# Kernel tuning notes

Measured on AMD Instinct MI355X. Metric: run time of the kernel, lower is better.

The kernel has to match this reference:

```python
import math
import jax, jax.numpy as jnp
import numpy as np

B, N, C = 4, 2048, 256
KMAX, RATIO, ITERS, H = 1024, 12.0, 3, 4
TAU, SIG_FLOOR, INIT_SIG_MIX, INIT_OFF, JIT = 1.0, 0.03, 0.1, 0.5, 1e-6
W_KL, W_ENT, W_OCC, W_COL = 0.05, 0.0, 0.5, 0.1
K_USE = min(max(1, math.ceil(N / RATIO)), KMAX)  # 171
EPS = 1e-8


def _sym(M):
    return 0.5 * (M + jnp.swapaxes(M, -1, -2))


def _l2n(x):
    return x / jnp.maximum(jnp.linalg.norm(x, axis=-1, keepdims=True), 1e-12)


def _ln(x, g, b):
    m = x.mean(-1, keepdims=True)
    v = ((x - m) ** 2).mean(-1, keepdims=True)
    return (x - m) / jnp.sqrt(v + 1e-5) * g + b


def setup_inputs():
    key = jax.random.key(0)
    ks = jax.random.split(key, 16)
    s = jax.random.normal(ks[0], (B, N, C), jnp.float32)
    mu = jax.random.normal(ks[1], (B, N, 3), jnp.float32)
    # per-point SPD covariances (Sigma must be PSD for the overlap solve)
    L = jax.random.normal(ks[2], (B, N, 3, 3), jnp.float32) * 0.3
    Sigma = L @ jnp.swapaxes(L, -1, -2) + 0.05 * jnp.eye(3, dtype=jnp.float32)
    mask = jnp.ones((B, N), jnp.float32)
    lim = 1.0 / math.sqrt(C)
    u = lambda k, sh: jax.random.uniform(k, sh, jnp.float32, -lim, lim)
    return dict(
        s=s, mu=mu, Sigma=Sigma, mask=mask,
        slot_embed_pool=jax.random.normal(ks[3], (KMAX, C), jnp.float32) * 0.02,
        geo_offsets_pool=jax.random.normal(ks[4], (KMAX, 3), jnp.float32) * 0.5,
        gating_W=u(ks[5], (C, C)), proj_q_W=u(ks[6], (C, C)), proj_k_W=u(ks[7], (C, C)),
        gru_w_ih=u(ks[8], (3 * C, C)), gru_w_hh=u(ks[9], (3 * C, C)),
        gru_b_ih=u(ks[10], (3 * C,)), gru_b_hh=u(ks[11], (3 * C,)),
        ln_g=jnp.ones((C,), jnp.float32), ln_b=jnp.zeros((C,), jnp.float32),
        mlp_w1=u(ks[12], (4 * C, C)), mlp_b1=u(ks[13], (4 * C,)),
        mlp_w2=u(ks[14], (C, 4 * C)), mlp_b2=u(ks[15], (C,)),
        w_geo=jnp.float32(1.0),
        geo_scale_raw=jnp.full((H,), -4.0, jnp.float32),
        geo_bias=jnp.full((H,), -6.0, jnp.float32),
    )


def _forward(s, mu, Sigma, mask, slot_embed_pool, geo_offsets_pool, gating_W,
             proj_q_W, proj_k_W, gru_w_ih, gru_w_hh, gru_b_ih, gru_b_hh,
             ln_g, ln_b, mlp_w1, mlp_b1, mlp_w2, mlp_b2,
             w_geo, geo_scale_raw, geo_bias):
    I3 = jnp.eye(3, dtype=s.dtype)
    m1 = mask[:, :, None]                    # [B,N,1]
    cnt = jnp.maximum(mask.sum(1), EPS)      # [B]

    # ---- slot selection (eval mode: no gate noise, rand_slots=0) ----
    s_global = (s * m1).sum(1) / cnt[:, None]
    q = _l2n(s_global @ gating_W.T)
    kn = _l2n(slot_embed_pool)
    scores = q @ kn.T                        # [B,KMAX]
    idx = jax.lax.top_k(scores, K_USE)[1]    # [B,K]
    slots = slot_embed_pool[idx]             # [B,K,C]
    geo_off = geo_offsets_pool[idx]          # [B,K,3]

    # ---- masked mean/std of mu ----
    mean = (mu * m1).sum(1) / cnt[:, None]   # [B,3]
    dm = mu - mean[:, None, :]
    cov = jnp.einsum('bni,bnj->bij', dm * m1, dm) / cnt[:, None, None]
    cov = _sym(cov)
    std = jnp.sqrt(jnp.maximum(jnp.diagonal(cov, axis1=-2, axis2=-1), EPS))
    std = jnp.maximum(std, SIG_FLOOR)
    mu_k = mean[:, None, :] + geo_off * (INIT_OFF * std[:, None, :])

    Sig_avg = _sym((Sigma * m1[..., None]).sum(1) / cnt[:, None, None])
    Sig_k = jnp.broadcast_to(Sig_avg[:, None] * INIT_SIG_MIX, (B, K_USE, 3, 3))
    Sig_k = Sig_k + (SIG_FLOOR ** 2) * I3 + JIT * I3

    k_sem = s @ proj_k_W.T                   # [B,N,C]
    a_h = jax.nn.softplus(geo_scale_raw)     # [H]
    A = None
    for _ in range(ITERS):
        q_sem = slots @ proj_q_W.T           # [B,K,C]
        logits_sem = jnp.einsum('bnc,bkc->bnk', k_sem, q_sem) / math.sqrt(C)
        delta = mu[:, :, None, :] - mu_k[:, None, :, :]       # [B,N,K,3]
        sig_sum = Sigma[:, :, None] + Sig_k[:, None]          # [B,N,K,3,3]
        sol = jnp.linalg.solve(sig_sum, delta[..., None])[..., 0]
        maha = (delta * sol).sum(-1)
        logdet = jnp.linalg.slogdet(sig_sum)[1]
        G = -0.5 * (maha + logdet)                            # [B,N,K]
        geo = (a_h[None, :, None, None] * G[:, None] + geo_bias[None, :, None, None]).sum(1)
        logits = (logits_sem + w_geo * geo) / max(TAU, 1e-6)
        logits = jnp.where(m1 < 0.5, -1e9, logits)
        A = jax.nn.softmax(logits, axis=-1) * m1              # [B,N,K]
        # moment-matching merge (A already mask-weighted; matches torch A*mask)
        occ = jnp.maximum(A.sum(1), EPS)                      # [B,K]
        mu_k = jnp.einsum('bnk,bni->bki', A, mu) / occ[..., None]
        d = mu[:, :, None, :] - mu_k[:, None, :, :]
        outer = d[..., :, None] * d[..., None, :]             # [B,N,K,3,3]
        Sig_k = (jnp.einsum('bnk,bnij->bkij', A, Sigma)
                 + jnp.einsum('bnk,bnkij->bkij', A, outer)) / occ[:, :, None, None]
        Sig_k = _sym(Sig_k) + max(JIT, 1e-6) * I3
        dg = jnp.diagonal(Sig_k, axis1=-2, axis2=-1)
        dg_f = jnp.maximum(dg, SIG_FLOOR ** 2)
        Sig_k = Sig_k - I3 * dg[..., None, :] + I3 * dg_f[..., None, :]
        Sig_k = _sym(Sig_k) + JIT * I3
        denom = jnp.maximum(A.sum(1), 1e-8)
        slot_in = jnp.einsum('bnk,bnc->bkc', A, s) / denom[..., None]
        # GRU cell
        x = slot_in.reshape(-1, C)
        h = slots.reshape(-1, C)
        gi = x @ gru_w_ih.T + gru_b_ih
        gh = h @ gru_w_hh.T + gru_b_hh
        r = jax.nn.sigmoid(gi[:, :C] + gh[:, :C])
        z = jax.nn.sigmoid(gi[:, C:2 * C] + gh[:, C:2 * C])
        n = jnp.tanh(gi[:, 2 * C:] + r * gh[:, 2 * C:])
        slots = ((1.0 - z) * n + z * h).reshape(B, K_USE, C)
        xm = _ln(slots, ln_g, ln_b)
        slots = slots + (jax.nn.gelu(xm @ mlp_w1.T + mlp_b1, approximate=False) @ mlp_w2.T + mlp_b2)

    # ---- losses ----
    hist = jnp.zeros((KMAX,), jnp.float32).at[idx.reshape(-1)].add(1.0)
    p = hist / jnp.maximum(hist.sum(), 1.0)
    pc = jnp.maximum(p, 1e-8)
    usage_kl = (pc * (jnp.log(pc) - math.log(1.0 / KMAX))).sum()
    usage_neg_ent = (pc * jnp.log(pc)).sum()
    occ2 = (A * m1).sum(1)
    occ2 = occ2 / jnp.maximum(occ2.sum(-1, keepdims=True), 1e-8)
    occ_mse = ((occ2 - 1.0 / K_USE) ** 2).mean()
    X = jnp.swapaxes(A * m1, 1, 2)           # [B,K,N]
    Xn = X / jnp.maximum(jnp.linalg.norm(X, axis=-1, keepdims=True), 1e-8)
    Gm = jnp.einsum('bkn,bln->bkl', Xn, Xn)
    eyeK = jnp.eye(K_USE, dtype=A.dtype)[None]
    off = (Gm - eyeK) * (1.0 - eyeK)
    col = (off ** 2).mean()
    total = W_KL * usage_kl + W_ENT * usage_neg_ent + W_OCC * occ_mse + W_COL * col
    return (A, slots, mu_k, Sig_k, idx, usage_kl, usage_neg_ent, occ_mse, col, total)


def reference(s, mu, Sigma, mask, slot_embed_pool, geo_offsets_pool, gating_W,
              proj_q_W, proj_k_W, gru_w_ih, gru_w_hh, gru_b_ih, gru_b_hh,
              ln_g, ln_b, mlp_w1, mlp_b1, mlp_w2, mlp_b2,
              w_geo, geo_scale_raw, geo_bias):
    return _forward(s, mu, Sigma, mask, slot_embed_pool, geo_offsets_pool, gating_W,
                    proj_q_W, proj_k_W, gru_w_ih, gru_w_hh, gru_b_ih, gru_b_hh,
                    ln_g, ln_b, mlp_w1, mlp_b1, mlp_w2, mlp_b2,
                    w_geo, geo_scale_raw, geo_bias)
```

## Files before the change

### kernel.cpp

```cpp
#include <hip/hip_runtime.h>
#include <math.h>

#define B_ 4
#define N_ 2048
#define C_ 256
#define KMAX_ 1024
#define KU_ 171
#define ITERS_ 3
#define H_ 4
#define EPS_ 1e-8f
#define SIGF_ 0.03f
#define JIT_ 1e-6f
#define LOGKMAX_ 6.93147180559945f

#define WS_CNT 0
#define WS_MUS 4
#define WS_MOS 16
#define WS_SGS 40
#define WS_COLACC 100
#define WS_SSUM 128
#define WS_STATS_BYTES (1152*4)
#define WS_MEAN 1152
#define WS_STD 1164
#define WS_SIGAVG 1176
#define WS_IDXI 1216
#define WS_KSEM 1920
#define WS_QSEM (WS_KSEM+2097152)
#define WS_OCC  (WS_QSEM+175104)
#define WS_PART (WS_OCC+704)
#define WS_TAIL (WS_PART+1400832)
#define WS_QV     WS_TAIL
#define WS_SCORE (WS_TAIL+1024)
#define WS_ACPART (WS_TAIL+8192)
#define WS_ATA (WS_TAIL+700416)

#define O_A 0
#define O_SLOTS 1400832
#define O_MUK   1575936
#define O_SIGK  1577988
#define O_IDX   1584144
#define O_KL    1584828
#define O_ENT   1584829
#define O_OCC   1584830
#define O_COL   1584831
#define O_TOT   1584832

__device__ __forceinline__ float wred(float v) {
  #pragma unroll
  for (int i = 32; i; i >>= 1) v += __shfl_xor(v, i);
  return v;
}
__device__ __forceinline__ float wmax(float v) {
  #pragma unroll
  for (int i = 32; i; i >>= 1) v = fmaxf(v, __shfl_xor(v, i));
  return v;
}

__device__ __forceinline__ float blk_red(float v, float* red, int t) {
  red[t] = v; __syncthreads();
  #pragma unroll
  for (int s = 128; s > 0; s >>= 1) {
    if (t < s) red[t] += red[t + s];
    __syncthreads();
  }
  float r = red[0]; __syncthreads();
  return r;
}

__global__ __launch_bounds__(256) void k_stats(const float* __restrict__ s,
    const float* __restrict__ mu, const float* __restrict__ Sigma,
    const float* __restrict__ mask, float* __restrict__ ws) {
  int blk = blockIdx.x; int b = blk / 8; int nc = blk % 8; int t = threadIdx.x;
  int n = nc * 256 + t;
  float m = mask[b * N_ + n];
  const float* mun = mu + ((size_t)(b * N_ + n)) * 3;
  float m0 = mun[0], m1v = mun[1], m2 = mun[2];
  const float* sgn = Sigma + ((size_t)(b * N_ + n)) * 9;
  float sg[9];
  #pragma unroll
  for (int j = 0; j < 9; j++) sg[j] = sgn[j];
  int lane = t & 63;
  float vals[19];
  vals[0] = m; vals[1] = m * m0; vals[2] = m * m1v; vals[3] = m * m2;
  vals[4] = m * m0 * m0; vals[5] = m * m0 * m1v; vals[6] = m * m0 * m2;
  vals[7] = m * m1v * m1v; vals[8] = m * m1v * m2; vals[9] = m * m2 * m2;
  #pragma unroll
  for (int j = 0; j < 9; j++) vals[10 + j] = m * sg[j];
  #pragma unroll
  for (int j = 0; j < 19; j++) {
    float v = wred(vals[j]);
    if (lane == 0) {
      int base = (j == 0) ? WS_CNT + b : (j < 4 ? WS_MUS + b * 3 + (j - 1)
                 : (j < 10 ? WS_MOS + b * 6 + (j - 4) : WS_SGS + b * 9 + (j - 10)));
      atomicAdd(ws + base, v);
    }
  }
  const float* sb = s + ((size_t)b * N_ + nc * 256) * C_;
  const float* mk = mask + b * N_ + nc * 256;
  float sa = 0.f;
  #pragma unroll 4
  for (int nn = 0; nn < 256; nn++) sa += mk[nn] * sb[(size_t)nn * C_ + t];
  atomicAdd(ws + WS_SSUM + b * C_ + t, sa);
}

__global__ __launch_bounds__(64) void k_fin(float* __restrict__ ws) {
  int t = threadIdx.x;
  if (t < B_) {
    int b = t;
    float cnt = fmaxf(ws[WS_CNT + b], EPS_);
    float me[3];
    #pragma unroll
    for (int i = 0; i < 3; i++) { me[i] = ws[WS_MUS + b * 3 + i] / cnt; ws[WS_MEAN + b * 3 + i] = me[i]; }
    const int dg[3] = {0, 3, 5};
    #pragma unroll
    for (int i = 0; i < 3; i++) {
      float cov = ws[WS_MOS + b * 6 + dg[i]] / cnt - me[i] * me[i];
      ws[WS_STD + b * 3 + i] = fmaxf(sqrtf(fmaxf(cov, EPS_)), SIGF_);
    }
    #pragma unroll
    for (int i = 0; i < 3; i++)
      #pragma unroll
      for (int j = 0; j < 3; j++)
        ws[WS_SIGAVG + b * 9 + i * 3 + j] =
            0.5f * (ws[WS_SGS + b * 9 + i * 3 + j] + ws[WS_SGS + b * 9 + j * 3 + i]) / cnt;
  }
}

__global__ __launch_bounds__(256) void k_qv(const float* __restrict__ ws_ssum,
    const float* __restrict__ gW, float* __restrict__ qv_o) {
  int b = blockIdx.x, t = threadIdx.x;
  __shared__ float sb[C_];
  __shared__ float rv[256];
  sb[t] = ws_ssum[b * C_ + t];
  __syncthreads();
  const float4* g4 = (const float4*)(gW + (size_t)t * C_);
  float qr = 0.f;
  #pragma unroll 4
  for (int c4 = 0; c4 < 64; c4++) {
    float4 g = g4[c4];
    qr += sb[c4 * 4] * g.x + sb[c4 * 4 + 1] * g.y + sb[c4 * 4 + 2] * g.z + sb[c4 * 4 + 3] * g.w;
  }
  float n2 = blk_red(qr * qr, rv, t);
  qv_o[b * C_ + t] = qr / fmaxf(sqrtf(n2), 1e-12f);
}

__global__ __launch_bounds__(256) void k_score(const float* __restrict__ qv,
    const float* __restrict__ pool, float* __restrict__ score) {
  int blk = blockIdx.x; int b = blk >> 4; int pc = blk & 15;
  int t = threadIdx.x; int row = pc * 64 + (t >> 2); int q = t & 3;
  __shared__ float qs[C_];
  qs[t] = qv[b * C_ + t];
  __syncthreads();
  const float4* p4 = (const float4*)(pool + (size_t)row * C_ + q * 64);
  float d = 0.f, p2 = 0.f;
  #pragma unroll
  for (int i = 0; i < 16; i++) {
    float4 pv = p4[i];
    int c = q * 64 + i * 4;
    d += qs[c] * pv.x + qs[c + 1] * pv.y + qs[c + 2] * pv.z + qs[c + 3] * pv.w;
    p2 += pv.x * pv.x + pv.y * pv.y + pv.z * pv.z + pv.w * pv.w;
  }
  d += __shfl_xor(d, 1); d += __shfl_xor(d, 2);
  p2 += __shfl_xor(p2, 1); p2 += __shfl_xor(p2, 2);
  if (q == 0) score[b * KMAX_ + row] = d / fmaxf(sqrtf(p2), 1e-12f);
}

__global__ __launch_bounds__(256) void k_sort(const float* __restrict__ score,
    int* __restrict__ idx_o, float* __restrict__ idxf_o) {
  int b = blockIdx.x, t = threadIdx.x;
  __shared__ float val[KMAX_]; __shared__ int id[KMAX_];
  for (int j = t; j < KMAX_; j += 256) { val[j] = score[b * KMAX_ + j]; id[j] = j; }
  __syncthreads();
  for (int kk = 2; kk <= KMAX_; kk <<= 1) {
    for (int j = kk >> 1; j > 0; j >>= 1) {
      for (int i = t; i < KMAX_; i += 256) {
        int ix = i ^ j;
        if (ix > i) {
          float va = val[i], vb = val[ix]; int ia = id[i], ib = id[ix];
          bool bBeforeA = (vb > va) || (vb == va && ib < ia);
          bool up = ((i & kk) == 0);
          if (up == bBeforeA) {
            val[i] = vb; val[ix] = va; id[i] = ib; id[ix] = ia;
          }
        }
      }
      __syncthreads();
    }
  }
  if (t < KU_) {
    idx_o[b * KU_ + t] = id[t];
    idxf_o[b * KU_ + t] = (float)id[t];
  }
}

__global__ __launch_bounds__(256) void k_init(const int* __restrict__ idx,
    const float* __restrict__ pool, const float* __restrict__ geop,
    const float* __restrict__ ws, float* __restrict__ slots,
    float* __restrict__ mu_k, float* __restrict__ sig_k) {
  int blk = blockIdx.x; int b = blk / KU_, k = blk % KU_; int t = threadIdx.x;
  int j = idx[b * KU_ + k];
  slots[((size_t)(b * KU_ + k)) * C_ + t] = pool[(size_t)j * C_ + t];
  if (t < 3) {
    mu_k[(b * KU_ + k) * 3 + t] = ws[WS_MEAN + b * 3 + t] + geop[j * 3 + t] * (0.5f * ws[WS_STD + b * 3 + t]);
  }
  if (t < 9) {
    float v = ws[WS_SIGAVG + b * 9 + t] * 0.1f;
    if (t == 0 || t == 4 || t == 8) v += SIGF_ * SIGF_ + JIT_;
    sig_k[((size_t)(b * KU_ + k)) * 9 + t] = v;
  }
}

template<int ROWS>
__global__ __launch_bounds__(256) void k_gemm_plain(const float* __restrict__ in,
    const float* __restrict__ W, float* __restrict__ out, int IN, int OUT, float scale) {
  extern __shared__ float sm[];
  int t = threadIdx.x; int r0 = blockIdx.x * ROWS;
  int C4 = IN >> 2;
  for (int i = t; i < ROWS * C4; i += 256) {
    int rr = i / C4;
    ((float4*)sm)[i] = ((const float4*)(in + (size_t)(r0 + rr) * IN))[i - rr * C4];
  }
  __syncthreads();
  const float4* W4 = (const float4*)(W + (size_t)t * IN);
  const float4* sm4 = (const float4*)sm;
  float acc[ROWS];
  #pragma unroll
  for (int a = 0; a < ROWS; a++) acc[a] = 0.f;
  for (int c4 = 0; c4 < C4; c4++) {
    float4 wv = W4[c4];
    #pragma unroll
    for (int a = 0; a < ROWS; a++) {
      float4 sv = sm4[a * C4 + c4];
      acc[a] += sv.x * wv.x + sv.y * wv.y + sv.z * wv.z + sv.w * wv.w;
    }
  }
  #pragma unroll
  for (int a = 0; a < ROWS; a++)
    out[(size_t)(r0 + a) * OUT + t] = acc[a] * scale;
}

__global__ __launch_bounds__(256) void k_lgsm(const float* __restrict__ ksem,
    const float* __restrict__ qsem, const float* __restrict__ mu,
    const float* __restrict__ Sigma, const float* __restrict__ mask,
    const float* __restrict__ mu_k, const float* __restrict__ sig_k,
    const float* __restrict__ wgeo, const float* __restrict__ gsr,
    const float* __restrict__ gbias, float* __restrict__ A) {
  __shared__ float ksm[16 * C_];
  __shared__ float Asm[16][172];
  __shared__ float muk[KU_ * 3];
  __shared__ float sgk[KU_ * 6];
  __shared__ float rowd[16][10];
  int blk = blockIdx.x; int b = blk / (N_ / 16); int nt = blk % (N_ / 16);
  int t = threadIdx.x; int r0 = nt * 16;
  for (int i = t; i < 16 * (C_ >> 2); i += 256) {
    int rr = i >> 6;
    ((float4*)ksm)[i] = ((const float4*)(ksem + ((size_t)(b * N_ + r0 + rr)) * C_))[i & 63];
  }
  for (int i = t; i < KU_ * 3; i += 256) muk[i] = mu_k[(size_t)b * KU_ * 3 + i];
  for (int i = t; i < KU_ * 6; i += 256) {
    int k = i / 6, c = i % 6;
    const int map[6] = {0, 1, 2, 4, 5, 8};
    sgk[i] = sig_k[((size_t)(b * KU_ + k)) * 9 + map[c]];
  }
  if (t < 160) {
    int rr = t / 10, c = t % 10;
    int n = r0 + rr;
    float v;
    if (c == 0) v = mask[b * N_ + n];
    else if (c < 4) v = mu[((size_t)(b * N_ + n)) * 3 + (c - 1)];
    else {
      const int map[6] = {0, 1, 2, 4, 5, 8};
      v = Sigma[((size_t)(b * N_ + n)) * 9 + map[c - 4]];
    }
    rowd[rr][c] = v;
  }
  __syncthreads();
  if (t < KU_) {
    const float4* q4 = (const float4*)(qsem + ((size_t)(b * KU_ + t)) * C_);
    const float4* sm4 = (const float4*)ksm;
    float acc[16];
    #pragma unroll
    for (int a = 0; a < 16; a++) acc[a] = 0.f;
    for (int c4 = 0; c4 < 64; c4++) {
      float4 qv = q4[c4];
      #pragma unroll
      for (int a = 0; a < 16; a++) {
        float4 sv = sm4[a * 64 + c4];
        acc[a] += sv.x * qv.x + sv.y * qv.y + sv.z * qv.z + sv.w * qv.w;
      }
    }
    float ah = 0.f, bs = 0.f;
    #pragma unroll
    for (int h = 0; h < H_; h++) {
      float x = gsr[h];
      ah += fmaxf(x, 0.f) + log1pf(expf(-fabsf(x)));
      bs += gbias[h];
    }
    float wg = wgeo[0];
    float mk0 = muk[t * 3], mk1 = muk[t * 3 + 1], mk2 = muk[t * 3 + 2];
    float k00 = sgk[t * 6], k01 = sgk[t * 6 + 1], k02 = sgk[t * 6 + 2];
    float k11 = sgk[t * 6 + 3], k12 = sgk[t * 6 + 4], k22 = sgk[t * 6 + 5];
    #pragma unroll
    for (int a = 0; a < 16; a++) {
      float m = rowd[a][0];
      float d0 = rowd[a][1] - mk0, d1 = rowd[a][2] - mk1, d2 = rowd[a][3] - mk2;
      float s00 = rowd[a][4] + k00, s01 = rowd[a][5] + k01, s02 = rowd[a][6] + k02;
      float s11 = rowd[a][7] + k11, s12 = rowd[a][8] + k12, s22 = rowd[a][9] + k22;
      float c00 = s11 * s22 - s12 * s12;
      float c01 = s02 * s12 - s01 * s22;
      float c02 = s01 * s12 - s02 * s11;
      float det = s00 * c00 + s01 * c01 + s02 * c02;
      float c11 = s00 * s22 - s02 * s02;
      float c12 = s01 * s02 - s00 * s12;
      float c22 = s00 * s11 - s01 * s01;
      float inv = 1.0f / det;
      float x0 = (c00 * d0 + c01 * d1 + c02 * d2) * inv;
      float x1 = (c01 * d0 + c11 * d1 + c12 * d2) * inv;
      float x2 = (c02 * d0 + c12 * d1 + c22 * d2) * inv;
      float maha = d0 * x0 + d1 * x1 + d2 * x2;
      float logdet = logf(fmaxf(det, 1e-30f));
      float G = -0.5f * (maha + logdet);
      float l = acc[a] * 0.0625f + wg * (ah * G + bs);
      if (m < 0.5f) l = -1e9f;
      Asm[a][t] = l;
    }
  }
  __syncthreads();
  int w = t >> 6, lane = t & 63;
  #pragma unroll
  for (int q = 0; q < 4; q++) {
    int a = w * 4 + q;
    float v0 = (lane < KU_) ? Asm[a][lane] : -INFINITY;
    float v1 = (lane + 64 < KU_) ? Asm[a][lane + 64] : -INFINITY;
    float v2 = (lane + 128 < KU_) ? Asm[a][lane + 128] : -INFINITY;
    float mx = wmax(fmaxf(v0, fmaxf(v1, v2)));
    float e0 = (lane < KU_) ? expf(v0 - mx) : 0.f;
    float e1 = (lane + 64 < KU_) ? expf(v1 - mx) : 0.f;
    float e2 = (lane + 128 < KU_) ? expf(v2 - mx) : 0.f;
    float ss = wred(e0 + e1 + e2);
    float scale = rowd[a][0] / ss;
    if (lane < KU_) Asm[a][lane] = e0 * scale;
    if (lane + 64 < KU_) Asm[a][lane + 64] = e1 * scale;
    if (lane + 128 < KU_) Asm[a][lane + 128] = e2 * scale;
  }
  __syncthreads();
  for (int i = t; i < 16 * KU_; i += 256) {
    int a = i / KU_, k = i - a * KU_;
    A[((size_t)(b * N_ + r0 + a)) * KU_ + k] = Asm[a][k];
  }
}

#define AC_NC 4
__global__ __launch_bounds__(256) void k_accum_part(const float* __restrict__ A,
    const float* __restrict__ mu, const float* __restrict__ Sigma,
    float* __restrict__ part) {
  int blk = blockIdx.x;
  int nc = blk & 3; int tmp = blk >> 2; int kt = tmp % 11; int b = tmp / 11;
  int t = threadIdx.x; int nn = t >> 4; int kk = t & 15;
  int k = kt * 16 + kk;
  float S[10];
  #pragma unroll
  for (int i = 0; i < 10; i++) S[i] = 0.f;
  __shared__ float rowd[16][10];
  const int NCH = N_ / AC_NC;
  for (int n0 = nc * NCH; n0 < nc * NCH + NCH; n0 += 16) {
    __syncthreads();
    if (t < 144) {
      int rr = t / 9, c = t % 9;
      int n = n0 + rr;
      float v;
      if (c < 3) v = mu[((size_t)(b * N_ + n)) * 3 + c];
      else {
        const int map[6] = {0, 1, 2, 4, 5, 8};
        v = Sigma[((size_t)(b * N_ + n)) * 9 + map[c - 3]];
      }
      rowd[rr][c] = v;
    }
    float a = (k < KU_) ? A[((size_t)(b * N_ + n0 + nn)) * KU_ + k] : 0.f;
    __syncthreads();
    float m0 = rowd[nn][0], m1 = rowd[nn][1], m2 = rowd[nn][2];
    float g0 = rowd[nn][3], g1 = rowd[nn][4], g2 = rowd[nn][5];
    float g4 = rowd[nn][6], g5 = rowd[nn][7], g8 = rowd[nn][8];
    S[0] += a; S[1] += a * m0; S[2] += a * m1; S[3] += a * m2;
    S[4] += a * (g0 + m0 * m0); S[5] += a * (g1 + m0 * m1); S[6] += a * (g2 + m0 * m2);
    S[7] += a * (g4 + m1 * m1); S[8] += a * (g5 + m1 * m2); S[9] += a * (g8 + m2 * m2);
  }
  #pragma unroll
  for (int i = 0; i < 10; i++) { S[i] += __shfl_xor(S[i], 16); S[i] += __shfl_xor(S[i], 32); }
  __shared__ float red[4][16][10];
  int w = t >> 6, lane = t & 63;
  if (lane < 16) {
    #pragma unroll
    for (int i = 0; i < 10; i++) red[w][lane][i] = S[i];
  }
  __syncthreads();
  if (t < 160) {
    int k2 = t / 10, i = t % 10;
    float v = red[0][k2][i] + red[1][k2][i] + red[2][k2][i] + red[3][k2][i];
    part[(((size_t)nc * B_ + b) * 176 + kt * 16 + k2) * 10 + i] = v;
  }
}

__global__ __launch_bounds__(256) void k_accum_fin(const float* __restrict__ part,
    float* __restrict__ occ, float* __restrict__ mu_k, float* __restrict__ sig_k) {
  int i = blockIdx.x * 256 + threadIdx.x;
  if (i >= B_ * KU_) return;
  int b = i / KU_, k = i % KU_;
  float p[10];
  #pragma unroll
  for (int j = 0; j < 10; j++) {
    float v = 0.f;
    #pragma unroll
    for (int nc = 0; nc < AC_NC; nc++)
      v += part[(((size_t)nc * B_ + b) * 176 + k) * 10 + j];
    p[j] = v;
  }
  float o = p[0];
  occ[b * KU_ + k] = o;
  float oc = fmaxf(o, EPS_);
  float s1x = p[1], s1y = p[2], s1z = p[3];
  float q0 = s1x / oc, q1 = s1y / oc, q2 = s1z / oc;
  mu_k[(b * KU_ + k) * 3 + 0] = q0;
  mu_k[(b * KU_ + k) * 3 + 1] = q1;
  mu_k[(b * KU_ + k) * 3 + 2] = q2;
  float v00 = (p[4] - 2.f * q0 * s1x + o * q0 * q0) / oc + JIT_;
  float v01 = (p[5] - q0 * s1y - s1x * q1 + o * q0 * q1) / oc;
  float v02 = (p[6] - q0 * s1z - s1x * q2 + o * q0 * q2) / oc;
  float v11 = (p[7] - 2.f * q1 * s1y + o * q1 * q1) / oc + JIT_;
  float v12 = (p[8] - q1 * s1z - s1y * q2 + o * q1 * q2) / oc;
  float v22 = (p[9] - 2.f * q2 * s1z + o * q2 * q2) / oc + JIT_;
  v00 = fmaxf(v00, SIGF_ * SIGF_) + JIT_;
  v11 = fmaxf(v11, SIGF_ * SIGF_) + JIT_;
  v22 = fmaxf(v22, SIGF_ * SIGF_) + JIT_;
  float* po = sig_k + ((size_t)(b * KU_ + k)) * 9;
  po[0] = v00; po[1] = v01; po[2] = v02;
  po[3] = v01; po[4] = v11; po[5] = v12;
  po[6] = v02; po[7] = v12; po[8] = v22;
}

__global__ __launch_bounds__(256) void k_atn_s(const float* __restrict__ A,
    const float* __restrict__ X, float* __restrict__ part) {
  int blk = blockIdx.x;
  int nc = blk & 7; int tmp = blk >> 3; int kt = tmp % 11; int b = tmp / 11;
  int t = threadIdx.x; int k0 = kt * 16;
  __shared__ float Ach[64 * 16];
  float acc[16];
  #pragma unroll
  for (int j = 0; j < 16; j++) acc[j] = 0.f;
  for (int n0 = nc * 256; n0 < nc * 256 + 256; n0 += 64) {
    __syncthreads();
    for (int i = t; i < 64 * 16; i += 256) {
      int nn = i >> 4, kk = i & 15; int k = k0 + kk;
      Ach[i] = (k < KU_) ? A[((size_t)(b * N_ + n0 + nn)) * KU_ + k] : 0.f;
    }
    __syncthreads();
    for (int nn = 0; nn < 64; nn++) {
      float xv = X[((size_t)(b * N_ + n0 + nn)) * C_ + t];
      #pragma unroll
      for (int j = 0; j < 16; j++) acc[j] += Ach[(nn << 4) + j] * xv;
    }
  }
  #pragma unroll
  for (int j = 0; j < 16; j++) {
    int k = k0 + j;
    if (k < KU_) part[((size_t)nc * (B_ * KU_) + b * KU_ + k) * C_ + t] = acc[j];
  }
}

__global__ __launch_bounds__(256) void k_atn(const float* __restrict__ A,
    const float* __restrict__ X, float* __restrict__ out, int NX) {
  int blk = blockIdx.x;
  int nc = blk & 7; int tmp = blk >> 3; int kt = tmp % 11; int b = tmp / 11;
  int t = threadIdx.x; int k0 = kt * 16;
  __shared__ float Ach[64 * 16];
  float acc[16];
  #pragma unroll
  for (int j = 0; j < 16; j++) acc[j] = 0.f;
  for (int n0 = nc * 256; n0 < nc * 256 + 256; n0 += 64) {
    __syncthreads();
    for (int i = t; i < 64 * 16; i += 256) {
      int nn = i >> 4, kk = i & 15; int k = k0 + kk;
      Ach[i] = (k < KU_) ? A[((size_t)(b * N_ + n0 + nn)) * KU_ + k] : 0.f;
    }
    __syncthreads();
    if (t < NX) {
      for (int nn = 0; nn < 64; nn++) {
        float xv = X[((size_t)(b * N_ + n0 + nn)) * NX + t];
        #pragma unroll
        for (int j = 0; j < 16; j++) acc[j] += Ach[(nn << 4) + j] * xv;
      }
    }
  }
  if (t < NX) {
    #pragma unroll
    for (int j = 0; j < 16; j++) {
      int k = k0 + j;
      if (k < KU_) atomicAdd(&out[((size_t)(b * KU_ + k)) * NX + t], acc[j]);
    }
  }
}

__global__ __launch_bounds__(256) void k_slotup(const float* __restrict__ part,
    const float* __restrict__ occ, float* __restrict__ slots,
    const float* __restrict__ wih, const float* __restrict__ bih,
    const float* __restrict__ whh, const float* __restrict__ bhh,
    const float* __restrict__ lng, const float* __restrict__ lnb,
    const float* __restrict__ w1p, const float* __restrict__ b1p,
    const float* __restrict__ w2p, const float* __restrict__ b2p,
    const float* __restrict__ qWp, float* __restrict__ qsem) {
  __shared__ float sx[1024], sh[1024], sg[1024], sxm[1024], shid[4096];
  int t = threadIdx.x; int r0 = blockIdx.x * 4;
  for (int i = t; i < 1024; i += 256) {
    int rr = i >> 8, c = i & 255;
    int r = r0 + rr;
    float v = 0.f;
    #pragma unroll
    for (int nc = 0; nc < 8; nc++) v += part[((size_t)nc * (B_ * KU_) + r) * C_ + c];
    sx[i] = v / fmaxf(occ[r], 1e-8f);
    sh[i] = slots[(size_t)r * C_ + c];
  }
  __syncthreads();
  {
    const float4* wir = (const float4*)(wih + (size_t)t * C_);
    const float4* wiz = (const float4*)(wih + (size_t)(t + 256) * C_);
    const float4* win = (const float4*)(wih + (size_t)(t + 512) * C_);
    const float4* whr = (const float4*)(whh + (size_t)t * C_);
    const float4* whz = (const float4*)(whh + (size_t)(t + 256) * C_);
    const float4* whn = (const float4*)(whh + (size_t)(t + 512) * C_);
    const float4* sx4 = (const float4*)sx;
    const float4* sh4 = (const float4*)sh;
    float gir[4] = {0,0,0,0}, giz[4] = {0,0,0,0}, gin[4] = {0,0,0,0};
    float ghr[4] = {0,0,0,0}, ghz[4] = {0,0,0,0}, ghn[4] = {0,0,0,0};
    for (int c4 = 0; c4 < 64; c4++) {
      float4 a1 = wir[c4], a2 = wiz[c4], a3 = win[c4];
      float4 h1 = whr[c4], h2 = whz[c4], h3 = whn[c4];
      #pragma unroll
      for (int a = 0; a < 4; a++) {
        float4 xv = sx4[a * 64 + c4], hv = sh4[a * 64 + c4];
        gir[a] += xv.x * a1.x + xv.y * a1.y + xv.z * a1.z + xv.w * a1.w;
        giz[a] += xv.x * a2.x + xv.y * a2.y + xv.z * a2.z + xv.w * a2.w;
        gin[a] += xv.x * a3.x + xv.y * a3.y + xv.z * a3.z + xv.w * a3.w;
        ghr[a] += hv.x * h1.x + hv.y * h1.y + hv.z * h1.z + hv.w * h1.w;
        ghz[a] += hv.x * h2.x + hv.y * h2.y + hv.z * h2.z + hv.w * h2.w;
        ghn[a] += hv.x * h3.x + hv.y * h3.y + hv.z * h3.z + hv.w * h3.w;
      }
    }
    float bir = bih[t], biz = bih[t + 256], bin = bih[t + 512];
    float bhr = bhh[t], bhz = bhh[t + 256], bhn = bhh[t + 512];
    #pragma unroll
    for (int a = 0; a < 4; a++) {
      float r = 1.f / (1.f + expf(-(gir[a] + bir + ghr[a] + bhr)));
      float z = 1.f / (1.f + expf(-(giz[a] + biz + ghz[a] + bhz)));
      float n = tanhf(gin[a] + bin + r * (ghn[a] + bhn));
      sg[a * 256 + t] = (1.f - z) * n + z * sh[a * 256 + t];
    }
  }
  __syncthreads();
  {
    int w = t >> 6, lane = t & 63;
    int a = w;
    float x0 = sg[a * 256 + lane], x1 = sg[a * 256 + lane + 64];
    float x2 = sg[a * 256 + lane + 128], x3 = sg[a * 256 + lane + 192];
    float mean = wred(x0 + x1 + x2 + x3) * (1.f / 256.f);
    float d0 = x0 - mean, d1 = x1 - mean, d2 = x2 - mean, d3 = x3 - mean;
    float var = wred(d0 * d0 + d1 * d1 + d2 * d2 + d3 * d3) * (1.f / 256.f);
    float rstd = rsqrtf(var + 1e-5f);
    sxm[a * 256 + lane]       = d0 * rstd * lng[lane]       + lnb[lane];
    sxm[a * 256 + lane + 64]  = d1 * rstd * lng[lane + 64]  + lnb[lane + 64];
    sxm[a * 256 + lane + 128] = d2 * rstd * lng[lane + 128] + lnb[lane + 128];
    sxm[a * 256 + lane + 192] = d3 * rstd * lng[lane + 192] + lnb[lane + 192];
  }
  __syncthreads();
  {
    const float4* q0 = (const float4*)(w1p + (size_t)t * C_);
    const float4* q1 = (const float4*)(w1p + (size_t)(t + 256) * C_);
    const float4* q2 = (const float4*)(w1p + (size_t)(t + 512) * C_);
    const float4* q3 = (const float4*)(w1p + (size_t)(t + 768) * C_);
    const float4* sxm4 = (const float4*)sxm;
    float acc[4][4];
    #pragma unroll
    for (int a = 0; a < 4; a++)
      #pragma unroll
      for (int j = 0; j < 4; j++) acc[a][j] = 0.f;
    for (int c4 = 0; c4 < 64; c4++) {
      float4 v0 = q0[c4], v1 = q1[c4], v2 = q2[c4], v3 = q3[c4];
      #pragma unroll
      for (int a = 0; a < 4; a++) {
        float4 xv = sxm4[a * 64 + c4];
        acc[a][0] += xv.x * v0.x + xv.y * v0.y + xv.z * v0.z + xv.w * v0.w;
        acc[a][1] += xv.x * v1.x + xv.y * v1.y + xv.z * v1.z + xv.w * v1.w;
        acc[a][2] += xv.x * v2.x + xv.y * v2.y + xv.z * v2.z + xv.w * v2.w;
        acc[a][3] += xv.x * v3.x + xv.y * v3.y + xv.z * v3.z + xv.w * v3.w;
      }
    }
    float bb0 = b1p[t], bb1 = b1p[t + 256], bb2v = b1p[t + 512], bb3 = b1p[t + 768];
    #pragma unroll
    for (int a = 0; a < 4; a++) {
      float v;
      v = acc[a][0] + bb0; shid[a * 1024 + t]       = 0.5f * v * (1.f + erff(v * 0.70710678118654752f));
      v = acc[a][1] + bb1; shid[a * 1024 + t + 256] = 0.5f * v * (1.f + erff(v * 0.70710678118654752f));
      v = acc[a][2] + bb2v; shid[a * 1024 + t + 512] = 0.5f * v * (1.f + erff(v * 0.70710678118654752f));
      v = acc[a][3] + bb3; shid[a * 1024 + t + 768] = 0.5f * v * (1.f + erff(v * 0.70710678118654752f));
    }
  }
  __syncthreads();
  {
    const float4* wr = (const float4*)(w2p + (size_t)t * 1024);
    const float4* sh4 = (const float4*)shid;
    float o[4] = {0, 0, 0, 0};
    for (int c4 = 0; c4 < 256; c4++) {
      float4 wv = wr[c4];
      #pragma unroll
      for (int a = 0; a < 4; a++) {
        float4 hv = sh4[a * 256 + c4];
        o[a] += hv.x * wv.x + hv.y * wv.y + hv.z * wv.z + hv.w * wv.w;
      }
    }
    float bb = b2p[t];
    #pragma unroll
    for (int a = 0; a < 4; a++) {
      float fin = sg[a * 256 + t] + o[a] + bb;
      slots[(size_t)(r0 + a) * C_ + t] = fin;
      sx[a * 256 + t] = fin;
    }
  }
  __syncthreads();
  {
    const float4* qr = (const float4*)(qWp + (size_t)t * C_);
    const float4* sx4 = (const float4*)sx;
    float o[4] = {0, 0, 0, 0};
    for (int c4 = 0; c4 < 64; c4++) {
      float4 wv = qr[c4];
      #pragma unroll
      for (int a = 0; a < 4; a++) {
        float4 xv = sx4[a * 64 + c4];
        o[a] += xv.x * wv.x + xv.y * wv.y + xv.z * wv.z + xv.w * wv.w;
      }
    }
    #pragma unroll
    for (int a = 0; a < 4; a++)
      qsem[(size_t)(r0 + a) * C_ + t] = o[a];
  }
}

__global__ __launch_bounds__(256) void k_hist(const int* __restrict__ idx,
    float* __restrict__ okl, float* __restrict__ oent) {
  __shared__ float hist[KMAX_];
  int t = threadIdx.x;
  for (int i = t; i < KMAX_; i += 256) hist[i] = 0.f;
  __syncthreads();
  for (int i = t; i < B_ * KU_; i += 256) atomicAdd(&hist[idx[i]], 1.0f);
  __syncthreads();
  float kl = 0.f, ent = 0.f;
  const float tot = (float)(B_ * KU_);
  for (int i = t; i < KMAX_; i += 256) {
    float pc = fmaxf(hist[i] / tot, 1e-8f);
    float lp = logf(pc);
    kl += pc * (lp + LOGKMAX_);
    ent += pc * lp;
  }
  __shared__ float red[256];
  kl = blk_red(kl, red, t); ent = blk_red(ent, red, t);
  if (t == 0) { okl[0] = kl; oent[0] = ent; }
}

__global__ __launch_bounds__(256) void k_occmse(const float* __restrict__ occ,
    float* __restrict__ out) {
  __shared__ float so[B_ * KU_];
  int t = threadIdx.x;
  for (int i = t; i < B_ * KU_; i += 256) so[i] = occ[i];
  __syncthreads();
  __shared__ float red[256];
  __shared__ float bsum[B_];
  for (int b = 0; b < B_; b++) {
    float s = 0.f;
    for (int i = t; i < KU_; i += 256) s += so[b * KU_ + i];
    s = blk_red(s, red, t);
    if (t == 0) bsum[b] = fmaxf(s, 1e-8f);
    __syncthreads();
  }
  float acc = 0.f;
  const float invK = 1.0f / (float)KU_;
  for (int i = t; i < B_ * KU_; i += 256) {
    int b = i / KU_;
    float v = so[i] / bsum[b] - invK;
    acc += v * v;
  }
  acc = blk_red(acc, red, t);
  if (t == 0) out[0] = acc / (float)(B_ * KU_);
}

__global__ __launch_bounds__(256) void k_colpart(const float* __restrict__ AtA,
    float* __restrict__ colacc) {
  int blk = blockIdx.x; int b = blk / KU_, k = blk % KU_; int t = threadIdx.x;
  float acc = 0.f;
  if (t < KU_ && t != k) {
    float dk = AtA[((size_t)(b * KU_ + k)) * KU_ + k];
    float dt = AtA[((size_t)(b * KU_ + t)) * KU_ + t];
    float v  = AtA[((size_t)(b * KU_ + k)) * KU_ + t];
    float gm = v / (fmaxf(sqrtf(dk), 1e-8f) * fmaxf(sqrtf(dt), 1e-8f));
    acc = gm * gm;
  }
  float v = wred(acc);
  __shared__ float p[4];
  if ((t & 63) == 0) p[t >> 6] = v;
  __syncthreads();
  if (t == 0) atomicAdd(colacc, p[0] + p[1] + p[2] + p[3]);
}

__global__ void k_colfin(const float* __restrict__ colacc,
    const float* __restrict__ okl, const float* __restrict__ oent,
    const float* __restrict__ oocc, float* __restrict__ ocol, float* __restrict__ otot) {
  float col = colacc[0] / (float)(B_ * KU_ * KU_);
  ocol[0] = col;
  otot[0] = 0.05f * okl[0] + 0.0f * oent[0] + 0.5f * oocc[0] + 0.1f * col;
}

extern "C" void kernel_launch(void* const* d_in, const int* in_sizes, int n_in,
                              void* d_out_v, int out_size, void* d_ws, size_t ws_size,
                              hipStream_t stream) {
  const float* s     = (const float*)d_in[0];
  const float* mu    = (const float*)d_in[1];
  const float* Sigma = (const float*)d_in[2];
  const float* mask  = (const float*)d_in[3];
  const float* pool  = (const float*)d_in[4];
  const float* geop  = (const float*)d_in[5];
  const float* gW    = (const float*)d_in[6];
  const float* qW    = (const float*)d_in[7];
  const float* kW    = (const float*)d_in[8];
  const float* wih   = (const float*)d_in[9];
  const float* whh   = (const float*)d_in[10];
  const float* bih   = (const float*)d_in[11];
  const float* bhh   = (const float*)d_in[12];
  const float* lng   = (const float*)d_in[13];
  const float* lnb   = (const float*)d_in[14];
  const float* w1    = (const float*)d_in[15];
  const float* b1    = (const float*)d_in[16];
  const float* w2    = (const float*)d_in[17];
  const float* b2    = (const float*)d_in[18];
  const float* wgeo  = (const float*)d_in[19];
  const float* gsr   = (const float*)d_in[20];
  const float* gbias = (const float*)d_in[21];

  float* out = (float*)d_out_v;
  float* A     = out + O_A;
  float* slots = out + O_SLOTS;
  float* muk   = out + O_MUK;
  float* sigk  = out + O_SIGK;
  float* idxf  = out + O_IDX;
  float* okl   = out + O_KL;
  float* oent  = out + O_ENT;
  float* oocc  = out + O_OCC;
  float* ocol  = out + O_COL;
  float* otot  = out + O_TOT;

  float* ws = (float*)d_ws;
  int*   idxi   = (int*)(ws + WS_IDXI);
  float* ksem   = ws + WS_KSEM;
  float* qsem   = ws + WS_QSEM;
  float* occ    = ws + WS_OCC;
  float* atpart = ws + WS_PART;
  float* acpart = ws + WS_ACPART;
  float* ata    = ws + WS_ATA;
  float* colacc = ws + WS_COLACC;

  hipMemsetAsync(ws, 0, WS_STATS_BYTES, stream);
  k_stats<<<B_ * 8, 256, 0, stream>>>(s, mu, Sigma, mask, ws);
  k_fin<<<1, 64, 0, stream>>>(ws);
  k_qv<<<B_, 256, 0, stream>>>(ws + WS_SSUM, gW, ws + WS_QV);
  k_score<<<B_ * 16, 256, 0, stream>>>(ws + WS_QV, pool, ws + WS_SCORE);
  k_sort<<<B_, 256, 0, stream>>>(ws + WS_SCORE, idxi, idxf);
  k_init<<<B_ * KU_, 256, 0, stream>>>(idxi, pool, geop, ws, slots, muk, sigk);

  k_gemm_plain<8><<<1024, 256, 8 * C_ * 4, stream>>>(s, kW, ksem, C_, C_, 1.0f);
  k_gemm_plain<4><<<171, 256, 4 * C_ * 4, stream>>>(slots, qW, qsem, C_, C_, 1.0f);

  for (int it = 0; it < ITERS_; ++it) {
    k_lgsm<<<B_ * (N_ / 16), 256, 0, stream>>>(ksem, qsem, mu, Sigma, mask,
                                               muk, sigk, wgeo, gsr, gbias, A);
    k_accum_part<<<B_ * 11 * AC_NC, 256, 0, stream>>>(A, mu, Sigma, acpart);
    k_accum_fin<<<3, 256, 0, stream>>>(acpart, occ, muk, sigk);
    k_atn_s<<<B_ * 11 * 8, 256, 0, stream>>>(A, s, atpart);
    k_slotup<<<171, 256, 0, stream>>>(atpart, occ, slots, wih, bih, whh, bhh,
                                      lng, lnb, w1, b1, w2, b2, qW, qsem);
  }

  hipMemsetAsync(ata, 0, (size_t)B_ * KU_ * KU_ * 4, stream);
  k_atn<<<B_ * 11 * 8, 256, 0, stream>>>(A, A, ata, KU_);
  k_colpart<<<B_ * KU_, 256, 0, stream>>>(ata, colacc);
  k_hist<<<1, 256, 0, stream>>>(idxi, okl, oent);
  k_occmse<<<1, 256, 0, stream>>>(occ, oocc);
  k_colfin<<<1, 1, 0, stream>>>(colacc, okl, oent, oocc, ocol, otot);
}
```

Before: 967.8 us.

## Split fused slot-update kernel into five parallel GRU/LN/MLP/query kernels

The single k_slotup kernel, which ran only 171 blocks each doing GRU gates, layernorm, a two-layer MLP and the query projection serially, is replaced by five kernels. Gate GEMMs, MLP layer 1 and the split-K MLP layer 2 now launch with 4x more blocks, with intermediates kept in workspace buffers. The goal is more parallelism across the GPU's compute units for the weight-bound matvecs. In exchange it adds launches and global round trips for the gate, hidden and partial-sum buffers, and it reuses the atpart workspace region for the layer-2 partials.

New measurement: 877.4 us. 9.3% less time.

```diff
diff --git a/kernel.cpp b/kernel.cpp
--- a/kernel.cpp
+++ b/kernel.cpp
@@ -6,6 +6,7 @@
 #define C_ 256
 #define KMAX_ 1024
 #define KU_ 171
+#define BK_ 684
 #define ITERS_ 3
 #define H_ 4
 #define EPS_ 1e-8f
@@ -28,11 +29,15 @@
 #define WS_QSEM (WS_KSEM+2097152)
 #define WS_OCC  (WS_QSEM+175104)
 #define WS_PART (WS_OCC+704)
-#define WS_TAIL (WS_PART+1400832)
-#define WS_QV     WS_TAIL
-#define WS_SCORE (WS_TAIL+1024)
-#define WS_ACPART (WS_TAIL+8192)
-#define WS_ATA (WS_TAIL+700416)
+#define WS_W2P  WS_PART
+#define WS_GBUF (WS_PART+1400832)
+#define WS_ATA  WS_GBUF
+#define WS_SNEW (WS_GBUF+700416)
+#define WS_XM   (WS_SNEW+175104)
+#define WS_HID  (WS_XM+175104)
+#define WS_ACPART (WS_HID+700416)
+#define WS_QV   (WS_ACPART+28160)
+#define WS_SCORE (WS_QV+1024)
 
 #define O_A 0
 #define O_SLOTS 1400832
@@ -500,147 +505,191 @@
   }
 }
 
-__global__ __launch_bounds__(256) void k_slotup(const float* __restrict__ part,
-    const float* __restrict__ occ, float* __restrict__ slots,
+__global__ __launch_bounds__(256) void k_gg(const float* __restrict__ part,
+    const float* __restrict__ occ, const float* __restrict__ slots,
     const float* __restrict__ wih, const float* __restrict__ bih,
     const float* __restrict__ whh, const float* __restrict__ bhh,
-    const float* __restrict__ lng, const float* __restrict__ lnb,
-    const float* __restrict__ w1p, const float* __restrict__ b1p,
-    const float* __restrict__ w2p, const float* __restrict__ b2p,
-    const float* __restrict__ qWp, float* __restrict__ qsem) {
-  __shared__ float sx[1024], sh[1024], sg[1024], sxm[1024], shid[4096];
-  int t = threadIdx.x; int r0 = blockIdx.x * 4;
-  for (int i = t; i < 1024; i += 256) {
+    float* __restrict__ gbuf) {
+  int p = blockIdx.y; int r0 = blockIdx.x * 8; int t = threadIdx.x;
+  __shared__ float sx[8 * C_];
+  __shared__ float sh[8 * C_];
+  bool needx = (p < 3), needh = (p != 2);
+  for (int i = t; i < 8 * C_; i += 256) {
     int rr = i >> 8, c = i & 255;
     int r = r0 + rr;
-    float v = 0.f;
-    #pragma unroll
-    for (int nc = 0; nc < 8; nc++) v += part[((size_t)nc * (B_ * KU_) + r) * C_ + c];
-    sx[i] = v / fmaxf(occ[r], 1e-8f);
-    sh[i] = slots[(size_t)r * C_ + c];
-  }
-  __syncthreads();
-  {
-    const float4* wir = (const float4*)(wih + (size_t)t * C_);
-    const float4* wiz = (const float4*)(wih + (size_t)(t + 256) * C_);
-    const float4* win = (const float4*)(wih + (size_t)(t + 512) * C_);
-    const float4* whr = (const float4*)(whh + (size_t)t * C_);
-    const float4* whz = (const float4*)(whh + (size_t)(t + 256) * C_);
-    const float4* whn = (const float4*)(whh + (size_t)(t + 512) * C_);
-    const float4* sx4 = (const float4*)sx;
-    const float4* sh4 = (const float4*)sh;
-    float gir[4] = {0,0,0,0}, giz[4] = {0,0,0,0}, gin[4] = {0,0,0,0};
-    float ghr[4] = {0,0,0,0}, ghz[4] = {0,0,0,0}, ghn[4] = {0,0,0,0};
+    if (r < BK_) {
+      if (needx) {
+        float v = 0.f;
+        #pragma unroll
+        for (int nc = 0; nc < 8; nc++) v += part[((size_t)nc * BK_ + r) * C_ + c];
+        sx[i] = v / fmaxf(occ[r], 1e-8f);
+      }
+      if (needh) sh[i] = slots[(size_t)r * C_ + c];
+    } else {
+      if (needx) sx[i] = 0.f;
+      if (needh) sh[i] = 0.f;
+    }
+  }
+  __syncthreads();
+  int grow = (p == 3) ? 512 + t : ((p == 2) ? 512 + t : p * 256 + t);
+  float acc[8];
+  #pragma unroll
+  for (int a = 0; a < 8; a++) acc[a] = 0.f;
+  const float4* sx4 = (const float4*)sx;
+  const float4* sh4 = (const float4*)sh;
+  if (p < 2) {
+    const float4* wi = (const float4*)(wih + (size_t)grow * C_);
+    const float4* wh = (const float4*)(whh + (size_t)grow * C_);
     for (int c4 = 0; c4 < 64; c4++) {
-      float4 a1 = wir[c4], a2 = wiz[c4], a3 = win[c4];
-      float4 h1 = whr[c4], h2 = whz[c4], h3 = whn[c4];
+      float4 a1 = wi[c4], a2 = wh[c4];
       #pragma unroll
-      for (int a = 0; a < 4; a++) {
+      for (int a = 0; a < 8; a++) {
         float4 xv = sx4[a * 64 + c4], hv = sh4[a * 64 + c4];
-        gir[a] += xv.x * a1.x + xv.y * a1.y + xv.z * a1.z + xv.w * a1.w;
-        giz[a] += xv.x * a2.x + xv.y * a2.y + xv.z * a2.z + xv.w * a2.w;
-        gin[a] += xv.x * a3.x + xv.y * a3.y + xv.z * a3.z + xv.w * a3.w;
-        ghr[a] += hv.x * h1.x + hv.y * h1.y + hv.z * h1.z + hv.w * h1.w;
-        ghz[a] += hv.x * h2.x + hv.y * h2.y + hv.z * h2.z + hv.w * h2.w;
-        ghn[a] += hv.x * h3.x + hv.y * h3.y + hv.z * h3.z + hv.w * h3.w;
+        acc[a] += xv.x * a1.x + xv.y * a1.y + xv.z * a1.z + xv.w * a1.w
+                + hv.x * a2.x + hv.y * a2.y + hv.z * a2.z + hv.w * a2.w;
       }
     }
-    float bir = bih[t], biz = bih[t + 256], bin = bih[t + 512];
-    float bhr = bhh[t], bhz = bhh[t + 256], bhn = bhh[t + 512];
+  } else if (p == 2) {
+    const float4* wi = (const float4*)(wih + (size_t)grow * C_);
+    for (int c4 = 0; c4 < 64; c4++) {
+      float4 a1 = wi[c4];
+      #pragma unroll
+      for (int a = 0; a < 8; a++) {
+        float4 xv = sx4[a * 64 + c4];
+        acc[a] += xv.x * a1.x + xv.y * a1.y + xv.z * a1.z + xv.w * a1.w;
+      }
+    }
+  } else {
+    const float4* wh = (const float4*)(whh + (size_t)grow * C_);
+    for (int c4 = 0; c4 < 64; c4++) {
+      float4 a2 = wh[c4];
+      #pragma unroll
+      for (int a = 0; a < 8; a++) {
+        float4 hv = sh4[a * 64 + c4];
+        acc[a] += hv.x * a2.x + hv.y * a2.y + hv.z * a2.z + hv.w * a2.w;
+      }
+    }
+  }
+  float bias = (p < 2) ? (bih[grow] + bhh[grow]) : ((p == 2) ? bih[grow] : bhh[grow]);
+  #pragma unroll
+  for (int a = 0; a < 8; a++) {
+    int r = r0 + a;
+    if (r < BK_) gbuf[((size_t)p * BK_ + r) * C_ + t] = acc[a] + bias;
+  }
+}
+
+__global__ __launch_bounds__(256) void k_gru_ln(const float* __restrict__ gbuf,
+    const float* __restrict__ slots, const float* __restrict__ lng,
+    const float* __restrict__ lnb, float* __restrict__ snew, float* __restrict__ xm) {
+  int r = blockIdx.x; int t = threadIdx.x;
+  float gr = gbuf[((size_t)0 * BK_ + r) * C_ + t];
+  float gz = gbuf[((size_t)1 * BK_ + r) * C_ + t];
+  float gi = gbuf[((size_t)2 * BK_ + r) * C_ + t];
+  float gh = gbuf[((size_t)3 * BK_ + r) * C_ + t];
+  float rg = 1.f / (1.f + expf(-gr));
+  float z = 1.f / (1.f + expf(-gz));
+  float n = tanhf(gi + rg * gh);
+  float h = slots[(size_t)r * C_ + t];
+  float sn = (1.f - z) * n + z * h;
+  snew[(size_t)r * C_ + t] = sn;
+  __shared__ float reda[4], redb[4];
+  int w = t >> 6, lane = t & 63;
+  float sum = wred(sn);
+  if (lane == 0) reda[w] = sum;
+  __syncthreads();
+  float mean = (reda[0] + reda[1] + reda[2] + reda[3]) * (1.f / 256.f);
+  float d = sn - mean;
+  float vs = wred(d * d);
+  if (lane == 0) redb[w] = vs;
+  __syncthreads();
+  float var = (redb[0] + redb[1] + redb[2] + redb[3]) * (1.f / 256.f);
+  xm[(size_t)r * C_ + t] = d * rsqrtf(var + 1e-5f) * lng[t] + lnb[t];
+}
+
+__global__ __launch_bounds__(256) void k_w1(const float* __restrict__ xm,
+    const float* __restrict__ w1p, const float* __restrict__ b1p,
+    float* __restrict__ hid) {
+  int r0 = blockIdx.x * 4; int t = threadIdx.x; int oc = blockIdx.y * 256 + t;
+  __shared__ float sm[4 * C_];
+  for (int i = t; i < 4 * 64; i += 256) {
+    int rr = i >> 6;
+    ((float4*)sm)[i] = ((const float4*)(xm + (size_t)(r0 + rr) * C_))[i & 63];
+  }
+  __syncthreads();
+  const float4* W4 = (const float4*)(w1p + (size_t)oc * C_);
+  const float4* sm4 = (const float4*)sm;
+  float acc[4] = {0, 0, 0, 0};
+  for (int c4 = 0; c4 < 64; c4++) {
+    float4 wv = W4[c4];
     #pragma unroll
     for (int a = 0; a < 4; a++) {
-      float r = 1.f / (1.f + expf(-(gir[a] + bir + ghr[a] + bhr)));
-      float z = 1.f / (1.f + expf(-(giz[a] + biz + ghz[a] + bhz)));
-      float n = tanhf(gin[a] + bin + r * (ghn[a] + bhn));
-      sg[a * 256 + t] = (1.f - z) * n + z * sh[a * 256 + t];
-    }
-  }
-  __syncthreads();
-  {
-    int w = t >> 6, lane = t & 63;
-    int a = w;
-    float x0 = sg[a * 256 + lane], x1 = sg[a * 256 + lane + 64];
-    float x2 = sg[a * 256 + lane + 128], x3 = sg[a * 256 + lane + 192];
-    float mean = wred(x0 + x1 + x2 + x3) * (1.f / 256.f);
-    float d0 = x0 - mean, d1 = x1 - mean, d2 = x2 - mean, d3 = x3 - mean;
-    float var = wred(d0 * d0 + d1 * d1 + d2 * d2 + d3 * d3) * (1.f / 256.f);
-    float rstd = rsqrtf(var + 1e-5f);
-    sxm[a * 256 + lane]       = d0 * rstd * lng[lane]       + lnb[lane];
-    sxm[a * 256 + lane + 64]  = d1 * rstd * lng[lane + 64]  + lnb[lane + 64];
-    sxm[a * 256 + lane + 128] = d2 * rstd * lng[lane + 128] + lnb[lane + 128];
-    sxm[a * 256 + lane + 192] = d3 * rstd * lng[lane + 192] + lnb[lane + 192];
-  }
-  __syncthreads();
-  {
-    const float4* q0 = (const float4*)(w1p + (size_t)t * C_);
-    const float4* q1 = (const float4*)(w1p + (size_t)(t + 256) * C_);
-    const float4* q2 = (const float4*)(w1p + (size_t)(t + 512) * C_);
-    const float4* q3 = (const float4*)(w1p + (size_t)(t + 768) * C_);
-    const float4* sxm4 = (const float4*)sxm;
-    float acc[4][4];
-    #pragma unroll
-    for (int a = 0; a < 4; a++)
-      #pragma unroll
-      for (int j = 0; j < 4; j++) acc[a][j] = 0.f;
-    for (int c4 = 0; c4 < 64; c4++) {
-      float4 v0 = q0[c4], v1 = q1[c4], v2 = q2[c4], v3 = q3[c4];
-      #pragma unroll
-      for (int a = 0; a < 4; a++) {
-        float4 xv = sxm4[a * 64 + c4];
-        acc[a][0] += xv.x * v0.x + xv.y * v0.y + xv.z * v0.z + xv.w * v0.w;
-        acc[a][1] += xv.x * v1.x + xv.y * v1.y + xv.z * v1.z + xv.w * v1.w;
-        acc[a][2] += xv.x * v2.x + xv.y * v2.y + xv.z * v2.z + xv.w * v2.w;
-        acc[a][3] += xv.x * v3.x + xv.y * v3.y + xv.z * v3.z + xv.w * v3.w;
-      }
-    }
-    float bb0 = b1p[t], bb1 = b1p[t + 256], bb2v = b1p[t + 512], bb3 = b1p[t + 768];
+      float4 sv = sm4[a * 64 + c4];
+      acc[a] += sv.x * wv.x + sv.y * wv.y + sv.z * wv.z + sv.w * wv.w;
+    }
+  }
+  float bb = b1p[oc];
+  #pragma unroll
+  for (int a = 0; a < 4; a++) {
+    float v = acc[a] + bb;
+    hid[(size_t)(r0 + a) * 1024 + oc] = 0.5f * v * (1.f + erff(v * 0.70710678118654752f));
+  }
+}
+
+__global__ __launch_bounds__(256) void k_w2p(const float* __restrict__ hid,
+    const float* __restrict__ w2p, float* __restrict__ w2part) {
+  int r0 = blockIdx.x * 4; int kc = blockIdx.y; int t = threadIdx.x;
+  __shared__ float sm[4 * C_];
+  for (int i = t; i < 4 * 64; i += 256) {
+    int rr = i >> 6;
+    ((float4*)sm)[i] = ((const float4*)(hid + (size_t)(r0 + rr) * 1024 + kc * 256))[i & 63];
+  }
+  __syncthreads();
+  const float4* W4 = (const float4*)(w2p + (size_t)t * 1024 + kc * 256);
+  const float4* sm4 = (const float4*)sm;
+  float acc[4] = {0, 0, 0, 0};
+  for (int c4 = 0; c4 < 64; c4++) {
+    float4 wv = W4[c4];
     #pragma unroll
     for (int a = 0; a < 4; a++) {
-      float v;
-      v = acc[a][0] + bb0; shid[a * 1024 + t]       = 0.5f * v * (1.f + erff(v * 0.70710678118654752f));
-      v = acc[a][1] + bb1; shid[a * 1024 + t + 256] = 0.5f * v * (1.f + erff(v * 0.70710678118654752f));
-      v = acc[a][2] + bb2v; shid[a * 1024 + t + 512] = 0.5f * v * (1.f + erff(v * 0.70710678118654752f));
-      v = acc[a][3] + bb3; shid[a * 1024 + t + 768] = 0.5f * v * (1.f + erff(v * 0.70710678118654752f));
-    }
-  }
-  __syncthreads();
-  {
-    const float4* wr = (const float4*)(w2p + (size_t)t * 1024);
-    const float4* sh4 = (const float4*)shid;
-    float o[4] = {0, 0, 0, 0};
-    for (int c4 = 0; c4 < 256; c4++) {
-      float4 wv = wr[c4];
-      #pragma unroll
-      for (int a = 0; a < 4; a++) {
-        float4 hv = sh4[a * 256 + c4];
-        o[a] += hv.x * wv.x + hv.y * wv.y + hv.z * wv.z + hv.w * wv.w;
-      }
-    }
-    float bb = b2p[t];
+      float4 sv = sm4[a * 64 + c4];
+      acc[a] += sv.x * wv.x + sv.y * wv.y + sv.z * wv.z + sv.w * wv.w;
+    }
+  }
+  #pragma unroll
+  for (int a = 0; a < 4; a++)
+    w2part[((size_t)kc * BK_ + r0 + a) * C_ + t] = acc[a];
+}
+
+__global__ __launch_bounds__(256) void k_qsemf(const float* __restrict__ snew,
+    const float* __restrict__ w2part, const float* __restrict__ b2p,
+    const float* __restrict__ qWp, float* __restrict__ slots,
+    float* __restrict__ qsem) {
+  int r0 = blockIdx.x * 4; int t = threadIdx.x;
+  __shared__ float sfin[4 * C_];
+  for (int i = t; i < 4 * C_; i += 256) {
+    int rr = i >> 8, c = i & 255;
+    int r = r0 + rr;
+    float v = snew[(size_t)r * C_ + c] + b2p[c];
+    #pragma unroll
+    for (int kc = 0; kc < 4; kc++) v += w2part[((size_t)kc * BK_ + r) * C_ + c];
+    sfin[i] = v;
+    slots[(size_t)r * C_ + c] = v;
+  }
+  __syncthreads();
+  const float4* qr = (const float4*)(qWp + (size_t)t * C_);
+  const float4* s4 = (const float4*)sfin;
+  float o[4] = {0, 0, 0, 0};
+  for (int c4 = 0; c4 < 64; c4++) {
+    float4 wv = qr[c4];
     #pragma unroll
     for (int a = 0; a < 4; a++) {
-      float fin = sg[a * 256 + t] + o[a] + bb;
-      slots[(size_t)(r0 + a) * C_ + t] = fin;
-      sx[a * 256 + t] = fin;
-    }
-  }
-  __syncthreads();
-  {
-    const float4* qr = (const float4*)(qWp + (size_t)t * C_);
-    const float4* sx4 = (const float4*)sx;
-    float o[4] = {0, 0, 0, 0};
-    for (int c4 = 0; c4 < 64; c4++) {
-      float4 wv = qr[c4];
-      #pragma unroll
-      for (int a = 0; a < 4; a++) {
-        float4 xv = sx4[a * 64 + c4];
-        o[a] += xv.x * wv.x + xv.y * wv.y + xv.z * wv.z + xv.w * wv.w;
-      }
-    }
-    #pragma unroll
-    for (int a = 0; a < 4; a++)
-      qsem[(size_t)(r0 + a) * C_ + t] = o[a];
-  }
+      float4 xv = s4[a * 64 + c4];
+      o[a] += xv.x * wv.x + xv.y * wv.y + xv.z * wv.z + xv.w * wv.w;
+    }
+  }
+  #pragma unroll
+  for (int a = 0; a < 4; a++)
+    qsem[(size_t)(r0 + a) * C_ + t] = o[a];
 }
 
 __global__ __launch_bounds__(256) void k_hist(const int* __restrict__ idx,
@@ -760,6 +809,11 @@
   float* qsem   = ws + WS_QSEM;
   float* occ    = ws + WS_OCC;
   float* atpart = ws + WS_PART;
+  float* gbuf   = ws + WS_GBUF;
+  float* snew   = ws + WS_SNEW;
+  float* xm     = ws + WS_XM;
+  float* hid    = ws + WS_HID;
+  float* w2part = ws + WS_W2P;
   float* acpart = ws + WS_ACPART;
   float* ata    = ws + WS_ATA;
   float* colacc = ws + WS_COLACC;
@@ -781,8 +835,11 @@
     k_accum_part<<<B_ * 11 * AC_NC, 256, 0, stream>>>(A, mu, Sigma, acpart);
     k_accum_fin<<<3, 256, 0, stream>>>(acpart, occ, muk, sigk);
     k_atn_s<<<B_ * 11 * 8, 256, 0, stream>>>(A, s, atpart);
-    k_slotup<<<171, 256, 0, stream>>>(atpart, occ, slots, wih, bih, whh, bhh,
-                                      lng, lnb, w1, b1, w2, b2, qW, qsem);
+    k_gg<<<dim3(86, 4), 256, 0, stream>>>(atpart, occ, slots, wih, bih, whh, bhh, gbuf);
+    k_gru_ln<<<BK_, 256, 0, stream>>>(gbuf, slots, lng, lnb, snew, xm);
+    k_w1<<<dim3(171, 4), 256, 0, stream>>>(xm, w1, b1, hid);
+    k_w2p<<<dim3(171, 4), 256, 0, stream>>>(hid, w2, w2part);
+    k_qsemf<<<171, 256, 0, stream>>>(snew, w2part, b2, qW, slots, qsem);
   }
 
   hipMemsetAsync(ata, 0, (size_t)B_ * KU_ * KU_ * 4, stream);
```
